# Kernel tuning notes

Measured on AMD Instinct MI355X. Metric: run time of the kernel, lower is better.

Reference implementation:

```python
import jax, jax.numpy as jnp
import numpy as np


def setup_inputs() -> dict:
    key = jax.random.key(0)
    ks = jax.random.split(key, 5)
    B, S, C, H = 32, 512, 320, 512
    scale = 1.0 / np.sqrt(H)
    return {
        "x": jax.random.normal(ks[0], (B, S, C), dtype=jnp.float32),
        "w_ih": jax.random.normal(ks[1], (4 * H, S), dtype=jnp.float32) * scale,
        "w_hh": jax.random.normal(ks[2], (4 * H, H), dtype=jnp.float32) * scale,
        "b_ih": jax.random.normal(ks[3], (4 * H,), dtype=jnp.float32) * scale,
        "b_hh": jax.random.normal(ks[4], (4 * H,), dtype=jnp.float32) * scale,
    }


def reference(x, w_ih, w_hh, b_ih, b_hh):
    # x: (B, S, C). Original permutes to (B, C, S) and runs a length-1 LSTM per
    # channel with zero initial state -> single LSTM cell step:
    #   gates = x_c @ W_ih^T + b_ih + b_hh   (W_hh @ h0 == 0)
    # PyTorch gate order: i, f, g, o.
    B, S, C = x.shape
    H = w_hh.shape[1]
    gates = jnp.einsum("bsc,gs->bcg", x, w_ih) + b_ih + b_hh  # (B, C, 4H)
    i_g, f_g, g_g, o_g = jnp.split(gates, 4, axis=-1)
    c = jax.nn.sigmoid(i_g) * jnp.tanh(g_g)           # c0 = 0
    h = jax.nn.sigmoid(o_g) * jnp.tanh(c)             # (B, C, H)
    # Faithful to torch: cat over channels along batch dim -> (C*B, H),
    # then reshape to (B, C, H) (scrambles batch/channel order).
    h = jnp.transpose(h, (1, 0, 2)).reshape(B, C, H)
    # dropout is identity in eval mode
    return jnp.transpose(h, (0, 2, 1))                # (B, H, C)
```

## Files before the change

kernel.cpp:

```cpp
#include <hip/hip_runtime.h>
#include <stdint.h>

#define B_  32
#define S_  512
#define C_  320
#define H_  512

typedef __attribute__((ext_vector_type(8))) short short8;
typedef __attribute__((ext_vector_type(4))) float f32x4;

__device__ __forceinline__ unsigned short f2bf(float x){
  unsigned u = __builtin_bit_cast(unsigned, x);
  u = u + 0x7FFFu + ((u >> 16) & 1u);
  return (unsigned short)(u >> 16);
}
__device__ __forceinline__ float bf2f(unsigned short h){
  unsigned u = ((unsigned)h) << 16;
  return __builtin_bit_cast(float, u);
}
__device__ __forceinline__ float sigf(float x){ return 1.0f/(1.0f + __expf(-x)); }
__device__ __forceinline__ float tanh_fast(float x){ return 2.0f/(1.0f + __expf(-2.0f*x)) - 1.0f; }

__device__ __forceinline__ void gload16(const void* g, void* l){
  __builtin_amdgcn_global_load_lds((const __attribute__((address_space(1))) void*)g,
                                   (__attribute__((address_space(3))) void*)l, 16, 0, 0);
}

__global__ __launch_bounds__(256) void k_cast_w(const float* __restrict__ w,
                                                unsigned short* __restrict__ wws){
  int idx = blockIdx.x*256 + threadIdx.x;
  float4 v = ((const float4*)w)[idx];
  uint2 p;
  p.x = (unsigned)f2bf(v.x) | ((unsigned)f2bf(v.y) << 16);
  p.y = (unsigned)f2bf(v.z) | ((unsigned)f2bf(v.w) << 16);
  ((uint2*)wws)[idx] = p;
}

__global__ __launch_bounds__(256) void k_cast_tx(const float* __restrict__ x,
                                                 unsigned short* __restrict__ xws){
  __shared__ float lds[64][65];
  const int tid = threadIdx.x;
  const int st = blockIdx.x, ctt = blockIdx.y, b = blockIdx.z;
  const int s0 = st*64, c0 = ctt*64;
  const int row = tid >> 2, q = tid & 3;

  const float* src = x + ((size_t)(b*S_ + s0 + row))*C_ + c0 + q*16;
  #pragma unroll
  for (int j = 0; j < 4; j++){
    float4 v = ((const float4*)src)[j];
    lds[row][q*16 + j*4 + 0] = v.x;
    lds[row][q*16 + j*4 + 1] = v.y;
    lds[row][q*16 + j*4 + 2] = v.z;
    lds[row][q*16 + j*4 + 3] = v.w;
  }
  __syncthreads();
  const int crow = row;
  #pragma unroll
  for (int j = 0; j < 2; j++){
    short8 o;
    #pragma unroll
    for (int e = 0; e < 8; e++)
      o[e] = (short)f2bf(lds[q*16 + j*8 + e][crow]);
    *(short8*)(xws + ((size_t)(b*C_ + c0 + crow))*S_ + s0 + q*16 + j*8) = o;
  }
}

__global__ __launch_bounds__(256) void k_gemm(const unsigned short* __restrict__ wws,
                                              const unsigned short* __restrict__ xws,
                                              const float* __restrict__ b_ih,
                                              const float* __restrict__ b_hh,
                                              unsigned short* __restrict__ hws){
  __shared__ alignas(16) char lds[2][32768];

  const int tid  = threadIdx.x;
  const int w    = tid >> 6;
  const int lane = tid & 63;
  const int kt = blockIdx.x, ct = blockIdx.y, b = blockIdx.z;
  const int k0 = kt*64, c0 = ct*64;

  f32x4 acc[3][4];
  #pragma unroll
  for (int gi = 0; gi < 3; gi++)
    #pragma unroll
    for (int nf = 0; nf < 4; nf++)
      acc[gi][nf] = (f32x4){0.f, 0.f, 0.f, 0.f};

  const int cr   = lane >> 3;
  const int slot = ((lane & 7) ^ cr) << 4;

  const char* srcp[8];
  char*       dstp[8];
  #pragma unroll
  for (int i = 0; i < 8; i++){
    int q = w*8 + i;
    if (q < 24){
      int gi = q >> 3, q8 = q & 7;
      int gr = (gi == 0 ? 0 : (gi == 1 ? 1024 : 1536));
      int grow = gr + k0 + q8*8 + cr;
      srcp[i] = (const char*)wws + ((size_t)grow*S_)*2 + slot;
      dstp[i] = &lds[0][0] + gi*8192 + q8*1024;
    } else {
      int q8 = q - 24;
      int xrow = b*C_ + c0 + q8*8 + cr;
      srcp[i] = (const char*)xws + ((size_t)xrow*S_)*2 + slot;
      dstp[i] = &lds[0][0] + 24576 + q8*1024;
    }
  }

  #pragma unroll
  for (int i = 0; i < 8; i++){ gload16(srcp[i], dstp[i]); srcp[i] += 128; }
  __syncthreads();

  const int arow = w*16 + (lane & 15);
  const int lo16 = (lane >> 4) << 4;
  const int swz  = (lane & 7) << 4;

  for (int t = 0; t < 8; t++){
    const int p = t & 1;
    if (t < 7){
      #pragma unroll
      for (int i = 0; i < 8; i++){
        gload16(srcp[i], dstp[i] + (p^1)*32768);
        srcp[i] += 128;
      }
    }
    const char* base = &lds[p][0];
    #pragma unroll
    for (int ks = 0; ks < 2; ks++){
      const int colb = (ks*64 + lo16) ^ swz;
      short8 aF[3], bF[4];
      #pragma unroll
      for (int gi = 0; gi < 3; gi++)
        aF[gi] = *(const short8*)(base + gi*8192 + arow*128 + colb);
      #pragma unroll
      for (int nf = 0; nf < 4; nf++){
        int brow = nf*16 + (lane & 15);
        bF[nf] = *(const short8*)(base + 24576 + brow*128 + colb);
      }
      #pragma unroll
      for (int gi = 0; gi < 3; gi++)
        #pragma unroll
        for (int nf = 0; nf < 4; nf++)
          acc[gi][nf] = __builtin_amdgcn_mfma_f32_16x16x32_bf16(aF[gi], bF[nf], acc[gi][nf], 0, 0, 0);
    }
    __syncthreads();
  }

  const int lkb = k0 + w*16 + ((lane >> 4) << 2);
  float bi[4], bg[4], bo[4];
  #pragma unroll
  for (int r = 0; r < 4; r++){
    bi[r] = b_ih[lkb + r]        + b_hh[lkb + r];
    bg[r] = b_ih[1024 + lkb + r] + b_hh[1024 + lkb + r];
    bo[r] = b_ih[1536 + lkb + r] + b_hh[1536 + lkb + r];
  }
  #pragma unroll
  for (int nf = 0; nf < 4; nf++){
    int c = c0 + nf*16 + (lane & 15);
    size_t n = (size_t)c*32 + (size_t)b;
    float h[4];
    #pragma unroll
    for (int r = 0; r < 4; r++){
      float iv = acc[0][nf][r] + bi[r];
      float gv = acc[1][nf][r] + bg[r];
      float ov = acc[2][nf][r] + bo[r];
      float cc = sigf(iv) * tanh_fast(gv);
      h[r] = sigf(ov) * tanh_fast(cc);
    }
    uint2 p2;
    p2.x = (unsigned)f2bf(h[0]) | ((unsigned)f2bf(h[1]) << 16);
    p2.y = (unsigned)f2bf(h[2]) | ((unsigned)f2bf(h[3]) << 16);
    *(uint2*)(hws + n*H_ + lkb) = p2;
  }
}

__global__ __launch_bounds__(256) void k_out(const unsigned short* __restrict__ hws,
                                             float* __restrict__ out){
  __shared__ float lds[64][65];
  const int tid = threadIdx.x;
  const int kt = blockIdx.x, ctt = blockIdx.y, b2 = blockIdx.z;
  const int k0 = kt*64, n0 = b2*320 + ctt*64;
  const int rr = tid >> 2, q = tid & 3;

  #pragma unroll
  for (int j = 0; j < 2; j++){
    short8 v = *(const short8*)(hws + ((size_t)(n0 + rr))*H_ + k0 + q*16 + j*8);
    #pragma unroll
    for (int e = 0; e < 8; e++)
      lds[rr][q*16 + j*8 + e] = bf2f((unsigned short)v[e]);
  }
  __syncthreads();
  const int krow = rr;
  #pragma unroll
  for (int j = 0; j < 4; j++){
    int c2l = q*16 + j*4;
    float4 o;
    o.x = lds[c2l + 0][krow];
    o.y = lds[c2l + 1][krow];
    o.z = lds[c2l + 2][krow];
    o.w = lds[c2l + 3][krow];
    *(float4*)(out + (size_t)b2*(H_*C_) + (size_t)(k0 + krow)*C_ + ctt*64 + c2l) = o;
  }
}

extern "C" void kernel_launch(void* const* d_in, const int* in_sizes, int n_in,
                              void* d_out, int out_size, void* d_ws, size_t ws_size,
                              hipStream_t stream){
  const float* x    = (const float*)d_in[0];
  const float* w_ih = (const float*)d_in[1];
  const float* b_ih = (const float*)d_in[3];
  const float* b_hh = (const float*)d_in[4];
  float* out = (float*)d_out;

  char* ws = (char*)d_ws;
  unsigned short* wws = (unsigned short*)(ws);
  unsigned short* xws = (unsigned short*)(ws + 2097152);
  unsigned short* hws = (unsigned short*)(ws + 2097152 + 10485760);

  k_cast_w <<<1024, 256, 0, stream>>>(w_ih, wws);
  k_cast_tx<<<dim3(8, 5, 32), 256, 0, stream>>>(x, xws);
  k_gemm   <<<dim3(8, 5, 32), 256, 0, stream>>>(wws, xws, b_ih, b_hh, hws);
  k_out    <<<dim3(8, 5, 32), 256, 0, stream>>>(hws, out);
}
```

Measured before the change: 59.03 us.

## Enlarge GEMM tile to cover all channels per block and compact gate weights

The gate GEMM now runs 512-thread blocks, each covering every one of the 320 channels for one batch and one 64-row hidden slice. This cuts the grid from 1280 to 256 blocks and reuses each loaded weight tile across all channels. Block indices are remapped so blocks that share a batch land on the same XCD. The weight cast kernel now packs only the three gate planes actually used (i, g, o), which drops the forget-gate conversion and simplifies row addressing in the GEMM. In exchange, each block needs 128KB of double-buffered LDS and holds many more accumulators, which limits occupancy to one block per CU and leaves only 256 blocks to fill the device.

```diff
diff --git a/kernel.cpp b/kernel.cpp
--- a/kernel.cpp
+++ b/kernel.cpp
@@ -5,6 +5,7 @@
 #define S_  512
 #define C_  320
 #define H_  512
+#define NROW (B_*C_)
 
 typedef __attribute__((ext_vector_type(8))) short short8;
 typedef __attribute__((ext_vector_type(4))) float f32x4;
@@ -27,13 +28,16 @@
 }
 
 __global__ __launch_bounds__(256) void k_cast_w(const float* __restrict__ w,
-                                                unsigned short* __restrict__ wws){
-  int idx = blockIdx.x*256 + threadIdx.x;
-  float4 v = ((const float4*)w)[idx];
+                                                unsigned short* __restrict__ aws){
+  int flat = blockIdx.x*256 + threadIdx.x;
+  int plane = flat >> 16;
+  int rem   = flat & 65535;
+  int srow  = (plane == 0 ? 0 : (plane == 1 ? 1024 : 1536));
+  float4 v = ((const float4*)w)[srow*128 + rem];
   uint2 p;
   p.x = (unsigned)f2bf(v.x) | ((unsigned)f2bf(v.y) << 16);
   p.y = (unsigned)f2bf(v.z) | ((unsigned)f2bf(v.w) << 16);
-  ((uint2*)wws)[idx] = p;
+  ((uint2*)aws)[flat] = p;
 }
 
 __global__ __launch_bounds__(256) void k_cast_tx(const float* __restrict__ x,
@@ -65,25 +69,32 @@
   }
 }
 
-__global__ __launch_bounds__(256) void k_gemm(const unsigned short* __restrict__ wws,
-                                              const unsigned short* __restrict__ xws,
-                                              const float* __restrict__ b_ih,
-                                              const float* __restrict__ b_hh,
-                                              unsigned short* __restrict__ hws){
-  __shared__ alignas(16) char lds[2][32768];
+__global__ __launch_bounds__(512, 2) void k_gemm(const unsigned short* __restrict__ aws,
+                                                 const unsigned short* __restrict__ xws,
+                                                 const float* __restrict__ b_ih,
+                                                 const float* __restrict__ b_hh,
+                                                 unsigned short* __restrict__ hws){
+  __shared__ alignas(16) char lds[2][65536];
 
   const int tid  = threadIdx.x;
   const int w    = tid >> 6;
   const int lane = tid & 63;
-  const int kt = blockIdx.x, ct = blockIdx.y, b = blockIdx.z;
-  const int k0 = kt*64, c0 = ct*64;
-
-  f32x4 acc[3][4];
+  const int wm = w >> 2, wn = w & 3;
+
+  const int flat = blockIdx.x;
+  const int xcd = flat & 7, j = flat >> 3;
+  const int b  = ((j >> 3) << 3) + xcd;
+  const int kt = j & 7;
+  const int k0 = kt*64;
+
+  f32x4 acc[3][2][5];
   #pragma unroll
   for (int gi = 0; gi < 3; gi++)
     #pragma unroll
-    for (int nf = 0; nf < 4; nf++)
-      acc[gi][nf] = (f32x4){0.f, 0.f, 0.f, 0.f};
+    for (int mf = 0; mf < 2; mf++)
+      #pragma unroll
+      for (int nf = 0; nf < 5; nf++)
+        acc[gi][mf][nf] = (f32x4){0.f, 0.f, 0.f, 0.f};
 
   const int cr   = lane >> 3;
   const int slot = ((lane & 7) ^ cr) << 4;
@@ -95,13 +106,12 @@
     int q = w*8 + i;
     if (q < 24){
       int gi = q >> 3, q8 = q & 7;
-      int gr = (gi == 0 ? 0 : (gi == 1 ? 1024 : 1536));
-      int grow = gr + k0 + q8*8 + cr;
-      srcp[i] = (const char*)wws + ((size_t)grow*S_)*2 + slot;
+      int grow = gi*512 + k0 + q8*8 + cr;
+      srcp[i] = (const char*)aws + ((size_t)grow*S_)*2 + slot;
       dstp[i] = &lds[0][0] + gi*8192 + q8*1024;
     } else {
       int q8 = q - 24;
-      int xrow = b*C_ + c0 + q8*8 + cr;
+      int xrow = b*C_ + q8*8 + cr;
       srcp[i] = (const char*)xws + ((size_t)xrow*S_)*2 + slot;
       dstp[i] = &lds[0][0] + 24576 + q8*1024;
     }
@@ -111,16 +121,16 @@
   for (int i = 0; i < 8; i++){ gload16(srcp[i], dstp[i]); srcp[i] += 128; }
   __syncthreads();
 
-  const int arow = w*16 + (lane & 15);
   const int lo16 = (lane >> 4) << 4;
   const int swz  = (lane & 7) << 4;
+  const int l15  = lane & 15;
 
   for (int t = 0; t < 8; t++){
     const int p = t & 1;
     if (t < 7){
       #pragma unroll
       for (int i = 0; i < 8; i++){
-        gload16(srcp[i], dstp[i] + (p^1)*32768);
+        gload16(srcp[i], dstp[i] + ((p^1) << 16));
         srcp[i] += 128;
       }
     }
@@ -128,49 +138,54 @@
     #pragma unroll
     for (int ks = 0; ks < 2; ks++){
       const int colb = (ks*64 + lo16) ^ swz;
-      short8 aF[3], bF[4];
-      #pragma unroll
-      for (int gi = 0; gi < 3; gi++)
-        aF[gi] = *(const short8*)(base + gi*8192 + arow*128 + colb);
-      #pragma unroll
-      for (int nf = 0; nf < 4; nf++){
-        int brow = nf*16 + (lane & 15);
-        bF[nf] = *(const short8*)(base + 24576 + brow*128 + colb);
-      }
+      short8 aF[3][2], bF[5];
       #pragma unroll
       for (int gi = 0; gi < 3; gi++)
         #pragma unroll
-        for (int nf = 0; nf < 4; nf++)
-          acc[gi][nf] = __builtin_amdgcn_mfma_f32_16x16x32_bf16(aF[gi], bF[nf], acc[gi][nf], 0, 0, 0);
+        for (int mf = 0; mf < 2; mf++)
+          aF[gi][mf] = *(const short8*)(base + gi*8192 + (wm*32 + mf*16 + l15)*128 + colb);
+      #pragma unroll
+      for (int nf = 0; nf < 5; nf++)
+        bF[nf] = *(const short8*)(base + 24576 + (wn*80 + nf*16 + l15)*128 + colb);
+      #pragma unroll
+      for (int gi = 0; gi < 3; gi++)
+        #pragma unroll
+        for (int mf = 0; mf < 2; mf++)
+          #pragma unroll
+          for (int nf = 0; nf < 5; nf++)
+            acc[gi][mf][nf] = __builtin_amdgcn_mfma_f32_16x16x32_bf16(aF[gi][mf], bF[nf], acc[gi][mf][nf], 0, 0, 0);
     }
     __syncthreads();
   }
 
-  const int lkb = k0 + w*16 + ((lane >> 4) << 2);
-  float bi[4], bg[4], bo[4];
-  #pragma unroll
-  for (int r = 0; r < 4; r++){
-    bi[r] = b_ih[lkb + r]        + b_hh[lkb + r];
-    bg[r] = b_ih[1024 + lkb + r] + b_hh[1024 + lkb + r];
-    bo[r] = b_ih[1536 + lkb + r] + b_hh[1536 + lkb + r];
-  }
-  #pragma unroll
-  for (int nf = 0; nf < 4; nf++){
-    int c = c0 + nf*16 + (lane & 15);
-    size_t n = (size_t)c*32 + (size_t)b;
-    float h[4];
+  #pragma unroll
+  for (int mf = 0; mf < 2; mf++){
+    const int kb = k0 + wm*32 + mf*16 + ((lane >> 4) << 2);
+    float bi[4], bg[4], bo[4];
     #pragma unroll
     for (int r = 0; r < 4; r++){
-      float iv = acc[0][nf][r] + bi[r];
-      float gv = acc[1][nf][r] + bg[r];
-      float ov = acc[2][nf][r] + bo[r];
-      float cc = sigf(iv) * tanh_fast(gv);
-      h[r] = sigf(ov) * tanh_fast(cc);
-    }
-    uint2 p2;
-    p2.x = (unsigned)f2bf(h[0]) | ((unsigned)f2bf(h[1]) << 16);
-    p2.y = (unsigned)f2bf(h[2]) | ((unsigned)f2bf(h[3]) << 16);
-    *(uint2*)(hws + n*H_ + lkb) = p2;
+      bi[r] = b_ih[kb + r]        + b_hh[kb + r];
+      bg[r] = b_ih[1024 + kb + r] + b_hh[1024 + kb + r];
+      bo[r] = b_ih[1536 + kb + r] + b_hh[1536 + kb + r];
+    }
+    #pragma unroll
+    for (int nf = 0; nf < 5; nf++){
+      const int c = wn*80 + nf*16 + l15;
+      const size_t n = (size_t)c*32 + (size_t)b;
+      float h[4];
+      #pragma unroll
+      for (int r = 0; r < 4; r++){
+        float iv = acc[0][mf][nf][r] + bi[r];
+        float gv = acc[1][mf][nf][r] + bg[r];
+        float ov = acc[2][mf][nf][r] + bo[r];
+        float cc = sigf(iv) * tanh_fast(gv);
+        h[r] = sigf(ov) * tanh_fast(cc);
+      }
+      uint2 p2;
+      p2.x = (unsigned)f2bf(h[0]) | ((unsigned)f2bf(h[1]) << 16);
+      p2.y = (unsigned)f2bf(h[2]) | ((unsigned)f2bf(h[3]) << 16);
+      *(uint2*)(hws + n*H_ + kb) = p2;
+    }
   }
 }
 
@@ -213,12 +228,12 @@
   float* out = (float*)d_out;
 
   char* ws = (char*)d_ws;
-  unsigned short* wws = (unsigned short*)(ws);
+  unsigned short* aws = (unsigned short*)(ws);
   unsigned short* xws = (unsigned short*)(ws + 2097152);
   unsigned short* hws = (unsigned short*)(ws + 2097152 + 10485760);
 
-  k_cast_w <<<1024, 256, 0, stream>>>(w_ih, wws);
+  k_cast_w <<<768, 256, 0, stream>>>(w_ih, aws);
   k_cast_tx<<<dim3(8, 5, 32), 256, 0, stream>>>(x, xws);
-  k_gemm   <<<dim3(8, 5, 32), 256, 0, stream>>>(wws, xws, b_ih, b_hh, hws);
+  k_gemm   <<<256, 512, 0, stream>>>(aws, xws, b_ih, b_hh, hws);
   k_out    <<<dim3(8, 5, 32), 256, 0, stream>>>(hws, out);
 }
```

Result: faster. 52.56 us (-11.0%).
